# Optimization experiments

Hardware: AMD Instinct MI355X
Metric: run time of the kernel (lower is better)

## Reference

```python
import jax, jax.numpy as jnp
import numpy as np

N_USERS = 50000
N_ITEMS = 50000
N_NODES = N_USERS + N_ITEMS
N_EDGES = 1600000
N_PAIRS = 200000
USER_DIM = 128
ITEM_DIM = 128
HID = 64
LAYER_NUM = 2


def setup_inputs() -> dict:
    key = jax.random.key(0)
    ks = jax.random.split(key, 16)
    inp = {
        "user_features": jax.random.normal(ks[0], (N_USERS, USER_DIM), jnp.float32),
        "item_features": jax.random.normal(ks[1], (N_ITEMS, ITEM_DIM), jnp.float32),
        "item_side_feat": jax.random.normal(ks[2], (N_ITEMS, HID), jnp.float32),
        "T_f": jax.random.uniform(ks[3], (2 * N_PAIRS,), jnp.float32),
        "T_cf": jax.random.uniform(ks[4], (2 * N_PAIRS,), jnp.float32),
        "Wu": jax.random.normal(ks[5], (USER_DIM, HID), jnp.float32) / np.sqrt(USER_DIM),
        "bu": jax.random.normal(ks[6], (HID,), jnp.float32) * 0.01,
        "Wi": jax.random.normal(ks[7], (ITEM_DIM, HID), jnp.float32) / np.sqrt(ITEM_DIM),
        "bi": jax.random.normal(ks[8], (HID,), jnp.float32) * 0.01,
        "W1": jax.random.normal(ks[9], (1 + 2 * HID, HID), jnp.float32) / np.sqrt(1 + 2 * HID),
        "b1": jax.random.normal(ks[10], (HID,), jnp.float32) * 0.01,
        "W2": jax.random.normal(ks[11], (HID, 1), jnp.float32) / np.sqrt(HID),
        "edge_src": jax.random.randint(ks[12], (N_EDGES,), 0, N_NODES, jnp.int32),
        "edge_dst": jax.random.randint(ks[13], (N_EDGES,), 0, N_NODES, jnp.int32),
        "userId": jax.random.randint(ks[14], (N_PAIRS,), 0, N_USERS, jnp.int32),
        "pos_itemId": jax.random.randint(ks[15], (N_PAIRS,), 0, N_ITEMS, jnp.int32),
        "neg_itemId": jax.random.randint(jax.random.fold_in(key, 99), (N_PAIRS,), 0, N_ITEMS, jnp.int32),
    }
    return inp


def reference(user_features, item_features, item_side_feat, T_f, T_cf,
              Wu, bu, Wi, bi, W1, b1, W2,
              edge_src, edge_dst, userId, pos_itemId, neg_itemId):
    # degree-based symmetric normalization (out_deg^-0.5 on src, in_deg^-0.5 on dst)
    ones = jnp.ones((edge_src.shape[0],), jnp.float32)
    out_deg = jax.ops.segment_sum(ones, edge_src, num_segments=N_NODES)
    in_deg = jax.ops.segment_sum(ones, edge_dst, num_segments=N_NODES)
    out_norm = jax.lax.rsqrt(jnp.clip(out_deg, 1.0))[:, None]  # [N,1]
    in_norm = jax.lax.rsqrt(jnp.clip(in_deg, 1.0))[:, None]

    def gcn_layer(node_f):
        m = node_f * out_norm                                   # [N,H]
        agg = jax.ops.segment_sum(m[edge_src], edge_dst, num_segments=N_NODES)
        return agg * in_norm

    user_embedding = jax.nn.relu(user_features @ Wu + bu)       # [Nu,H]
    item_embedding = jax.nn.relu(item_features @ Wi + bi)       # [Ni,H]

    for i in range(LAYER_NUM):
        if i == 0:
            embeddings = gcn_layer(jnp.concatenate([user_embedding, item_embedding], axis=0))
        else:
            embeddings = gcn_layer(embeddings)
        scale = 1.0 / (i + 2)
        user_embedding = user_embedding + embeddings[:N_USERS] * scale
        item_embedding = item_embedding + embeddings[N_USERS:] * scale

    item_embedding = item_embedding + item_side_feat

    userE = user_embedding[userId]                              # [P,H]
    posE = item_embedding[pos_itemId]
    negE = item_embedding[neg_itemId]
    zi = jnp.concatenate([userE, userE], axis=0)                # [2P,H]
    zj = jnp.concatenate([posE, negE], axis=0)

    def decode(T):
        h = jnp.concatenate([zi, zj, T[:, None]], axis=1)       # [2P, 2H+1]
        h = jax.nn.elu(h @ W1 + b1)
        return (h @ W2)[:, 0]                                   # [2P]

    logits_f = decode(T_f)
    logits_cf = decode(T_cf)
    return (user_embedding, item_embedding, logits_f, logits_cf)
```

## Files before the change

kernel.cpp:

```cpp
#include <hip/hip_runtime.h>

#define NU 50000
#define NI 50000
#define NN 100000
#define NE 1600000
#define NP 200000
#define DIM 128
#define HID 64

#define HR 4
#define HC 32
#define RN (NN / HR)
#define RNW (RN / 2)
#define CE (NE / HC)

typedef unsigned short bf16_t;
typedef __attribute__((ext_vector_type(8))) short short8;
typedef __attribute__((ext_vector_type(4))) float f32x4;

__device__ __forceinline__ float bf2f(unsigned short u) {
  union { unsigned int i; float f; } c; c.i = ((unsigned int)u) << 16; return c.f;
}
__device__ __forceinline__ unsigned short f2bf(float f) {
  union { float f; unsigned int i; } c; c.f = f;
  unsigned int i = c.i;
  i += 0x7fffu + ((i >> 16) & 1u);
  return (unsigned short)(i >> 16);
}
__device__ __forceinline__ int geti(const void* p, int i, bool i64) {
  return i64 ? (int)((const long long*)p)[i] : ((const int*)p)[i];
}

__global__ __launch_bounds__(64) void k_detect(const bf16_t* __restrict__ uf,
                                               const int* __restrict__ ei,
                                               int* __restrict__ flag) {
  int lane = threadIdx.x;
  float m = 0.f;
  for (int i = lane; i < 4096; i += 64) {
    float v = fabsf(bf2f(uf[i]));
    if (v < 3e38f) m = fmaxf(m, v);
  }
  int cnt = 0;
  for (int i = lane; i < 4096; i += 64) {
    if (ei[2 * i + 1] == 0) cnt++;
  }
  for (int off = 32; off > 0; off >>= 1) {
    m = fmaxf(m, __shfl_xor(m, off));
    cnt += __shfl_xor(cnt, off);
  }
  if (lane == 0) {
    flag[0] = (m > 100.f) ? 1 : 0;
    flag[1] = (cnt > 2048) ? 1 : 0;
  }
}

__global__ __launch_bounds__(1024) void k_hist(const void* __restrict__ srcv,
                                               const void* __restrict__ dstv,
                                               const int* __restrict__ flag,
                                               int* __restrict__ pout,
                                               int* __restrict__ pin) {
  __shared__ unsigned int ho[RNW];
  __shared__ unsigned int hd[RNW];
  const bool i64 = (flag[1] != 0);
  int r = blockIdx.x & (HR - 1);
  int c = blockIdx.x >> 2;
  int lo = r * RN, hiN = lo + RN;
  int t = threadIdx.x;
  for (int i = t; i < RNW; i += 1024) { ho[i] = 0u; hd[i] = 0u; }
  __syncthreads();
  int ebeg = c * CE;
  if (!i64) {
    const int* sp = (const int*)srcv + ebeg;
    const int* dp = (const int*)dstv + ebeg;
    for (int e = t * 4; e < CE; e += 1024 * 4) {
      int4 sv = *(const int4*)(sp + e);
      int4 dv = *(const int4*)(dp + e);
      int ss[4] = {sv.x, sv.y, sv.z, sv.w};
      int dd[4] = {dv.x, dv.y, dv.z, dv.w};
#pragma unroll
      for (int k = 0; k < 4; ++k) {
        int s = ss[k];
        if (s >= lo && s < hiN) {
          int loc = s - lo;
          atomicAdd(&ho[loc >> 1], 1u << ((loc & 1) * 16));
        }
        int d = dd[k];
        if (d >= lo && d < hiN) {
          int loc = d - lo;
          atomicAdd(&hd[loc >> 1], 1u << ((loc & 1) * 16));
        }
      }
    }
  } else {
    const long long* sp = (const long long*)srcv + ebeg;
    const long long* dp = (const long long*)dstv + ebeg;
    for (int e = t; e < CE; e += 1024) {
      int s = (int)sp[e];
      if (s >= lo && s < hiN) {
        int loc = s - lo;
        atomicAdd(&ho[loc >> 1], 1u << ((loc & 1) * 16));
      }
      int d = (int)dp[e];
      if (d >= lo && d < hiN) {
        int loc = d - lo;
        atomicAdd(&hd[loc >> 1], 1u << ((loc & 1) * 16));
      }
    }
  }
  __syncthreads();
  int* po = pout + c * NN + lo;
  int* pi = pin + c * NN + lo;
  for (int i = t; i < RNW; i += 1024) {
    unsigned int o = ho[i], d = hd[i];
    int2 ov; ov.x = (int)(o & 0xffffu); ov.y = (int)(o >> 16);
    int2 dv; dv.x = (int)(d & 0xffffu); dv.y = (int)(d >> 16);
    *(int2*)(po + 2 * i) = ov;
    *(int2*)(pi + 2 * i) = dv;
  }
}

__global__ __launch_bounds__(256) void k_reduce(const int* __restrict__ pout,
                                                int* __restrict__ pin,
                                                int* __restrict__ din,
                                                float* __restrict__ onorm,
                                                float* __restrict__ inorm) {
  int n = blockIdx.x * 256 + threadIdx.x;
  if (n >= NN) return;
  int so = 0;
#pragma unroll
  for (int c = 0; c < HC; ++c) so += pout[c * NN + n];
  int si = 0;
#pragma unroll
  for (int c = 0; c < HC; ++c) {
    int v = pin[c * NN + n];
    pin[c * NN + n] = si;
    si += v;
  }
  din[n] = si;
  onorm[n] = rsqrtf((float)(so > 1 ? so : 1));
  inorm[n] = rsqrtf((float)(si > 1 ? si : 1));
}

__global__ __launch_bounds__(256) void k_scan1(const int* __restrict__ in,
                                               int* __restrict__ bsums, int n) {
  __shared__ int sh[256];
  int t = threadIdx.x;
  int base = blockIdx.x * 1024 + t * 4;
  int s = 0;
#pragma unroll
  for (int i = 0; i < 4; ++i)
    if (base + i < n) s += in[base + i];
  sh[t] = s;
  __syncthreads();
  for (int off = 128; off > 0; off >>= 1) {
    if (t < off) sh[t] += sh[t + off];
    __syncthreads();
  }
  if (t == 0) bsums[blockIdx.x] = sh[0];
}

__global__ __launch_bounds__(128) void k_scan2(const int* __restrict__ bsums,
                                               int* __restrict__ boffs, int nb) {
  __shared__ int sh[128];
  int t = threadIdx.x;
  int own = (t < nb) ? bsums[t] : 0;
  sh[t] = own;
  __syncthreads();
  for (int off = 1; off < 128; off <<= 1) {
    int add = (t >= off) ? sh[t - off] : 0;
    __syncthreads();
    sh[t] += add;
    __syncthreads();
  }
  if (t < nb) boffs[t] = sh[t] - own;
}

__global__ __launch_bounds__(256) void k_scan3(const int* __restrict__ in,
                                               const int* __restrict__ boffs,
                                               int* __restrict__ row_ptr, int n) {
  __shared__ int sh[256];
  int t = threadIdx.x;
  int base = blockIdx.x * 1024 + t * 4;
  int v[4];
  int s = 0;
#pragma unroll
  for (int i = 0; i < 4; ++i) {
    v[i] = (base + i < n) ? in[base + i] : 0;
    s += v[i];
  }
  sh[t] = s;
  __syncthreads();
  for (int off = 1; off < 256; off <<= 1) {
    int add = (t >= off) ? sh[t - off] : 0;
    __syncthreads();
    sh[t] += add;
    __syncthreads();
  }
  int excl = boffs[blockIdx.x] + sh[t] - s;
#pragma unroll
  for (int i = 0; i < 4; ++i) {
    if (base + i < n) {
      row_ptr[base + i] = excl;
      excl += v[i];
    }
  }
  if (blockIdx.x == 0 && t == 0) row_ptr[n] = NE;
}

__global__ __launch_bounds__(1024) void k_fill2(const void* __restrict__ srcv,
                                                const void* __restrict__ dstv,
                                                const int* __restrict__ flag,
                                                const int* __restrict__ row_ptr,
                                                const int* __restrict__ pin,
                                                int* __restrict__ csr_src) {
  __shared__ int cur[RN];
  const bool i64 = (flag[1] != 0);
  int r = blockIdx.x & (HR - 1);
  int c = blockIdx.x >> 2;
  int lo = r * RN, hiN = lo + RN;
  int t = threadIdx.x;
  const int* pi = pin + c * NN + lo;
  const int* rp = row_ptr + lo;
  for (int i = t; i < RN; i += 1024) cur[i] = rp[i] + pi[i];
  __syncthreads();
  int ebeg = c * CE;
  if (!i64) {
    const int* sp = (const int*)srcv + ebeg;
    const int* dp = (const int*)dstv + ebeg;
    for (int e = t * 4; e < CE; e += 1024 * 4) {
      int4 dv = *(const int4*)(dp + e);
      int4 sv = *(const int4*)(sp + e);
      int dd[4] = {dv.x, dv.y, dv.z, dv.w};
      int ss[4] = {sv.x, sv.y, sv.z, sv.w};
#pragma unroll
      for (int k = 0; k < 4; ++k) {
        int d = dd[k];
        if (d >= lo && d < hiN) {
          int slot = atomicAdd(&cur[d - lo], 1);
          csr_src[slot] = ss[k];
        }
      }
    }
  } else {
    const long long* sp = (const long long*)srcv + ebeg;
    const long long* dp = (const long long*)dstv + ebeg;
    for (int e = t; e < CE; e += 1024) {
      int d = (int)dp[e];
      if (d >= lo && d < hiN) {
        int slot = atomicAdd(&cur[d - lo], 1);
        csr_src[slot] = (int)sp[e];
      }
    }
  }
}

__global__ __launch_bounds__(256) void k_embed(const void* __restrict__ featv,
                                               const void* __restrict__ Wv,
                                               const void* __restrict__ biasv,
                                               const int* __restrict__ flag,
                                               const float* __restrict__ onorm_base,
                                               float* __restrict__ out,
                                               bf16_t* __restrict__ embs, int rows) {
  __shared__ float Ws[DIM * HID];
  __shared__ float bs[HID];
  const bool f32 = (flag[0] != 0);
  int t = threadIdx.x;
  if (f32) {
    const float* W = (const float*)Wv;
    for (int i = t; i < DIM * HID; i += 256) Ws[i] = W[i];
    if (t < HID) bs[t] = ((const float*)biasv)[t];
  } else {
    const bf16_t* W = (const bf16_t*)Wv;
    for (int i = t; i < DIM * HID; i += 256) Ws[i] = bf2f(W[i]);
    if (t < HID) bs[t] = bf2f(((const bf16_t*)biasv)[t]);
  }
  __syncthreads();
  int rl = t >> 4;
  int jq = t & 15;
  for (int rbase = blockIdx.x * 16; rbase < rows; rbase += gridDim.x * 16) {
    int row = rbase + rl;
    if (row >= rows) continue;
    float a0 = 0.f, a1 = 0.f, a2 = 0.f, a3 = 0.f;
    if (f32) {
      const float* fr = (const float*)featv + (size_t)row * DIM;
      for (int k0 = 0; k0 < DIM; k0 += 4) {
        float4 f4 = *(const float4*)(fr + k0);
        float fk[4] = {f4.x, f4.y, f4.z, f4.w};
#pragma unroll
        for (int kk = 0; kk < 4; ++kk) {
          const float* wr = &Ws[(k0 + kk) * HID + jq * 4];
          a0 += fk[kk] * wr[0];
          a1 += fk[kk] * wr[1];
          a2 += fk[kk] * wr[2];
          a3 += fk[kk] * wr[3];
        }
      }
    } else {
      const bf16_t* fr = (const bf16_t*)featv + (size_t)row * DIM;
      for (int k0 = 0; k0 < DIM; k0 += 8) {
        uint4 u = *(const uint4*)(fr + k0);
        unsigned int w[4] = {u.x, u.y, u.z, u.w};
#pragma unroll
        for (int kk = 0; kk < 8; ++kk) {
          unsigned short us = (unsigned short)((w[kk >> 1] >> ((kk & 1) * 16)) & 0xffffu);
          float fk = bf2f(us);
          const float* wr = &Ws[(k0 + kk) * HID + jq * 4];
          a0 += fk * wr[0];
          a1 += fk * wr[1];
          a2 += fk * wr[2];
          a3 += fk * wr[3];
        }
      }
    }
    float4 r;
    r.x = fmaxf(a0 + bs[jq * 4 + 0], 0.f);
    r.y = fmaxf(a1 + bs[jq * 4 + 1], 0.f);
    r.z = fmaxf(a2 + bs[jq * 4 + 2], 0.f);
    r.w = fmaxf(a3 + bs[jq * 4 + 3], 0.f);
    *(float4*)&out[(size_t)row * HID + jq * 4] = r;
    float sc = onorm_base[row];
    uint2 p;
    p.x = (unsigned int)f2bf(r.x * sc) | ((unsigned int)f2bf(r.y * sc) << 16);
    p.y = (unsigned int)f2bf(r.z * sc) | ((unsigned int)f2bf(r.w * sc) << 16);
    *(uint2*)&embs[(size_t)row * HID + jq * 4] = p;
  }
}

__global__ __launch_bounds__(256) void k_gather1(const bf16_t* __restrict__ embs,
                                                 const float* __restrict__ onorm,
                                                 const float* __restrict__ inorm,
                                                 const int* __restrict__ row_ptr,
                                                 const int* __restrict__ csr_src,
                                                 bf16_t* __restrict__ e1s) {
  int n = blockIdx.x * 4 + (threadIdx.x >> 6);
  if (n >= NN) return;
  int lane = threadIdx.x & 63;
  int g = lane >> 3;
  int l8 = (lane & 7) * 8;
  int beg = row_ptr[n], end = row_ptr[n + 1];
  float a[8];
#pragma unroll
  for (int j = 0; j < 8; ++j) a[j] = 0.f;
  for (int base = beg; base < end; base += 32) {
    int ev[4], sv[4];
#pragma unroll
    for (int k = 0; k < 4; ++k) {
      int ee = base + k * 8 + g;
      ev[k] = ee;
      sv[k] = csr_src[ee < end ? ee : end - 1];
    }
#pragma unroll
    for (int k = 0; k < 4; ++k) {
      uint4 u = *(const uint4*)(embs + (size_t)sv[k] * HID + l8);
      bool valid = ev[k] < end;
      unsigned int w[4] = {u.x, u.y, u.z, u.w};
#pragma unroll
      for (int j = 0; j < 4; ++j) {
        unsigned int wj = valid ? w[j] : 0u;
        a[2 * j]     += bf2f((unsigned short)(wj & 0xffffu));
        a[2 * j + 1] += bf2f((unsigned short)(wj >> 16));
      }
    }
  }
#pragma unroll
  for (int j = 0; j < 8; ++j) {
    a[j] += __shfl_xor(a[j], 8);
    a[j] += __shfl_xor(a[j], 16);
    a[j] += __shfl_xor(a[j], 32);
  }
  if (g == 0) {
    float sc = inorm[n] * onorm[n];
    uint4 p;
    p.x = (unsigned int)f2bf(a[0] * sc) | ((unsigned int)f2bf(a[1] * sc) << 16);
    p.y = (unsigned int)f2bf(a[2] * sc) | ((unsigned int)f2bf(a[3] * sc) << 16);
    p.z = (unsigned int)f2bf(a[4] * sc) | ((unsigned int)f2bf(a[5] * sc) << 16);
    p.w = (unsigned int)f2bf(a[6] * sc) | ((unsigned int)f2bf(a[7] * sc) << 16);
    *(uint4*)(e1s + (size_t)n * HID + l8) = p;
  }
}

__global__ __launch_bounds__(256) void k_gather2c(float* __restrict__ emb0,
                                                  const bf16_t* __restrict__ e1s,
                                                  const void* __restrict__ sidev,
                                                  const int* __restrict__ flag,
                                                  const float* __restrict__ onorm,
                                                  const float* __restrict__ inorm,
                                                  const int* __restrict__ row_ptr,
                                                  const int* __restrict__ csr_src,
                                                  bf16_t* __restrict__ fin_bf) {
  int n = blockIdx.x * 4 + (threadIdx.x >> 6);
  if (n >= NN) return;
  int lane = threadIdx.x & 63;
  int g = lane >> 3;
  int l8 = (lane & 7) * 8;
  int beg = row_ptr[n], end = row_ptr[n + 1];
  float a[8];
#pragma unroll
  for (int j = 0; j < 8; ++j) a[j] = 0.f;
  for (int base = beg; base < end; base += 32) {
    int ev[4], sv[4];
#pragma unroll
    for (int k = 0; k < 4; ++k) {
      int ee = base + k * 8 + g;
      ev[k] = ee;
      sv[k] = csr_src[ee < end ? ee : end - 1];
    }
#pragma unroll
    for (int k = 0; k < 4; ++k) {
      uint4 u = *(const uint4*)(e1s + (size_t)sv[k] * HID + l8);
      bool valid = ev[k] < end;
      unsigned int w[4] = {u.x, u.y, u.z, u.w};
#pragma unroll
      for (int j = 0; j < 4; ++j) {
        unsigned int wj = valid ? w[j] : 0u;
        a[2 * j]     += bf2f((unsigned short)(wj & 0xffffu));
        a[2 * j + 1] += bf2f((unsigned short)(wj >> 16));
      }
    }
  }
#pragma unroll
  for (int j = 0; j < 8; ++j) {
    a[j] += __shfl_xor(a[j], 8);
    a[j] += __shfl_xor(a[j], 16);
    a[j] += __shfl_xor(a[j], 32);
  }
  if (g == 0) {
    float inorm_n = inorm[n];
    float inv_on = 1.0f / onorm[n];
    size_t off = (size_t)n * HID + l8;
    uint4 u = *(const uint4*)(e1s + off);
    unsigned int w[4] = {u.x, u.y, u.z, u.w};
    float e1v[8];
#pragma unroll
    for (int j = 0; j < 4; ++j) {
      e1v[2 * j]     = bf2f((unsigned short)(w[j] & 0xffffu)) * inv_on;
      e1v[2 * j + 1] = bf2f((unsigned short)(w[j] >> 16)) * inv_on;
    }
    float4 b0 = *(const float4*)&emb0[off];
    float4 b1 = *(const float4*)&emb0[off + 4];
    float bb[8] = {b0.x, b0.y, b0.z, b0.w, b1.x, b1.y, b1.z, b1.w};
    const float s2 = 1.f / 3.f;
    float vv[8];
#pragma unroll
    for (int j = 0; j < 8; ++j)
      vv[j] = bb[j] + 0.5f * e1v[j] + s2 * a[j] * inorm_n;
    if (n >= NU) {
      size_t soff = (size_t)(n - NU) * HID + l8;
      if (flag[0] != 0) {
        float4 s0 = *(const float4*)((const float*)sidev + soff);
        float4 s1 = *(const float4*)((const float*)sidev + soff + 4);
        vv[0] += s0.x; vv[1] += s0.y; vv[2] += s0.z; vv[3] += s0.w;
        vv[4] += s1.x; vv[5] += s1.y; vv[6] += s1.z; vv[7] += s1.w;
      } else {
        uint4 su = *(const uint4*)((const bf16_t*)sidev + soff);
        unsigned int sw[4] = {su.x, su.y, su.z, su.w};
#pragma unroll
        for (int j = 0; j < 4; ++j) {
          vv[2 * j]     += bf2f((unsigned short)(sw[j] & 0xffffu));
          vv[2 * j + 1] += bf2f((unsigned short)(sw[j] >> 16));
        }
      }
    }
    float4 o0, o1;
    o0.x = vv[0]; o0.y = vv[1]; o0.z = vv[2]; o0.w = vv[3];
    o1.x = vv[4]; o1.y = vv[5]; o1.z = vv[6]; o1.w = vv[7];
    *(float4*)&emb0[off] = o0;
    *(float4*)&emb0[off + 4] = o1;
    uint4 pb;
    pb.x = (unsigned int)f2bf(vv[0]) | ((unsigned int)f2bf(vv[1]) << 16);
    pb.y = (unsigned int)f2bf(vv[2]) | ((unsigned int)f2bf(vv[3]) << 16);
    pb.z = (unsigned int)f2bf(vv[4]) | ((unsigned int)f2bf(vv[5]) << 16);
    pb.w = (unsigned int)f2bf(vv[6]) | ((unsigned int)f2bf(vv[7]) << 16);
    *(uint4*)(fin_bf + off) = pb;
  }
}

__global__ __launch_bounds__(256) void k_decode(const bf16_t* __restrict__ zb,
                                                const void* __restrict__ W1v,
                                                const void* __restrict__ b1v,
                                                const void* __restrict__ W2v,
                                                const void* __restrict__ Tfv,
                                                const void* __restrict__ Tcfv,
                                                const int* __restrict__ flag,
                                                const void* __restrict__ userId,
                                                const void* __restrict__ posId,
                                                const void* __restrict__ negId,
                                                float* __restrict__ out_lf,
                                                float* __restrict__ out_lcf) {
  __shared__ bf16_t W1b[128 * 65];
  __shared__ float wlast[HID], b1s[HID], W2s[HID];
  const bool f32 = (flag[0] != 0);
  const bool i64 = (flag[1] != 0);
  int t = threadIdx.x;
  if (f32) {
    const float* W1 = (const float*)W1v;
    for (int i = t; i < 128 * 64; i += 256) W1b[(i >> 6) * 65 + (i & 63)] = f2bf(W1[i]);
    if (t < HID) {
      wlast[t] = W1[128 * 64 + t];
      b1s[t] = ((const float*)b1v)[t];
      W2s[t] = ((const float*)W2v)[t];
    }
  } else {
    const bf16_t* W1 = (const bf16_t*)W1v;
    for (int i = t; i < 128 * 64; i += 256) W1b[(i >> 6) * 65 + (i & 63)] = W1[i];
    if (t < HID) {
      wlast[t] = bf2f(W1[128 * 64 + t]);
      b1s[t] = bf2f(((const bf16_t*)b1v)[t]);
      W2s[t] = bf2f(((const bf16_t*)W2v)[t]);
    }
  }
  __syncthreads();
  int wv = t >> 6;
  int lane = t & 63;
  int m = lane & 15;
  int q = lane >> 4;
  short8 Bf[4][4];
#pragma unroll
  for (int c = 0; c < 4; ++c)
#pragma unroll
    for (int nt = 0; nt < 4; ++nt)
#pragma unroll
      for (int j = 0; j < 8; ++j)
        Bf[c][nt][j] = (short)W1b[(c * 32 + q * 8 + j) * 65 + nt * 16 + m];

  const int tiles = (2 * NP) / 16;
  for (int tile = blockIdx.x * 4 + wv; tile < tiles; tile += gridDim.x * 4) {
    int pr = tile * 16 + m;
    int pid = pr < NP ? pr : pr - NP;
    int uid = geti(userId, pid, i64);
    int iid = (pr < NP) ? geti(posId, pid, i64) : geti(negId, pid, i64);
    const bf16_t* ur = zb + (size_t)uid * HID;
    const bf16_t* ir = zb + (size_t)(NU + iid) * HID;
    short8 a0 = *(const short8*)(ur + q * 8);
    short8 a1 = *(const short8*)(ur + 32 + q * 8);
    short8 a2 = *(const short8*)(ir + q * 8);
    short8 a3 = *(const short8*)(ir + 32 + q * 8);
    f32x4 acc[4];
#pragma unroll
    for (int nt = 0; nt < 4; ++nt) acc[nt] = (f32x4)(0.f);
#pragma unroll
    for (int nt = 0; nt < 4; ++nt) {
      acc[nt] = __builtin_amdgcn_mfma_f32_16x16x32_bf16(a0, Bf[0][nt], acc[nt], 0, 0, 0);
      acc[nt] = __builtin_amdgcn_mfma_f32_16x16x32_bf16(a1, Bf[1][nt], acc[nt], 0, 0, 0);
      acc[nt] = __builtin_amdgcn_mfma_f32_16x16x32_bf16(a2, Bf[2][nt], acc[nt], 0, 0, 0);
      acc[nt] = __builtin_amdgcn_mfma_f32_16x16x32_bf16(a3, Bf[3][nt], acc[nt], 0, 0, 0);
    }
    float tfr[4], tcfr[4];
    int rbase = tile * 16 + q * 4;
    if (f32) {
      float4 t4 = *(const float4*)((const float*)Tfv + rbase);
      float4 c4 = *(const float4*)((const float*)Tcfv + rbase);
      tfr[0] = t4.x; tfr[1] = t4.y; tfr[2] = t4.z; tfr[3] = t4.w;
      tcfr[0] = c4.x; tcfr[1] = c4.y; tcfr[2] = c4.z; tcfr[3] = c4.w;
    } else {
      const bf16_t* tp = (const bf16_t*)Tfv + rbase;
      const bf16_t* cp = (const bf16_t*)Tcfv + rbase;
#pragma unroll
      for (int r = 0; r < 4; ++r) { tfr[r] = bf2f(tp[r]); tcfr[r] = bf2f(cp[r]); }
    }
#pragma unroll
    for (int r = 0; r < 4; ++r) {
      float sf = 0.f, scf = 0.f;
#pragma unroll
      for (int nt = 0; nt < 4; ++nt) {
        int n = nt * 16 + m;
        float x = acc[nt][r] + b1s[n];
        float wl = wlast[n];
        float w2 = W2s[n];
        float bfv = x + tfr[r] * wl;
        float bcv = x + tcfr[r] * wl;
        float hf = bfv > 0.f ? bfv : (__expf(bfv) - 1.f);
        float hc = bcv > 0.f ? bcv : (__expf(bcv) - 1.f);
        sf += hf * w2;
        scf += hc * w2;
      }
      sf += __shfl_xor(sf, 1); scf += __shfl_xor(scf, 1);
      sf += __shfl_xor(sf, 2); scf += __shfl_xor(scf, 2);
      sf += __shfl_xor(sf, 4); scf += __shfl_xor(scf, 4);
      sf += __shfl_xor(sf, 8); scf += __shfl_xor(scf, 8);
      if (m == 0) {
        int pr2 = rbase + r;
        out_lf[pr2] = sf;
        out_lcf[pr2] = scf;
      }
    }
  }
}

extern "C" void kernel_launch(void* const* d_in, const int* in_sizes, int n_in,
                              void* d_out, int out_size, void* d_ws, size_t ws_size,
                              hipStream_t stream) {
  (void)in_sizes; (void)n_in; (void)out_size;
  const void* user_f = d_in[0];
  const void* item_f = d_in[1];
  const void* side   = d_in[2];
  const void* Tf     = d_in[3];
  const void* Tcf    = d_in[4];
  const void* Wu     = d_in[5];
  const void* bu     = d_in[6];
  const void* Wi     = d_in[7];
  const void* bi     = d_in[8];
  const void* W1     = d_in[9];
  const void* b1     = d_in[10];
  const void* W2     = d_in[11];
  const void* esrc   = d_in[12];
  const void* edst   = d_in[13];
  const void* userId = d_in[14];
  const void* posId  = d_in[15];
  const void* negId  = d_in[16];

  const size_t WS_NEEDED = 33601280;
  if (ws_size < WS_NEEDED) return;

  char* ws = (char*)d_ws;
  int*   deg_in  = (int*)(ws + 0);
  float* onorm   = (float*)(ws + 400000);
  float* inorm   = (float*)(ws + 800000);
  int*   row_ptr = (int*)(ws + 1200000);
  int*   bsums   = (int*)(ws + 1600128);
  int*   boffs   = (int*)(ws + 1600640);
  int*   flag    = (int*)(ws + 1601152);
  int*   csr_src = (int*)(ws + 1601280);
  int*   pout    = (int*)(ws + 8001280);
  int*   pin     = (int*)(ws + 20801280);
  bf16_t* embs   = (bf16_t*)(ws + 8001280);
  bf16_t* e1s    = (bf16_t*)(ws + 20801280);
  bf16_t* fin_bf = embs;

  float* out     = (float*)d_out;
  float* emb0    = out;
  float* out_lf  = out + (size_t)NN * HID;
  float* out_lcf = out_lf + 2 * NP;

  k_detect<<<1, 64, 0, stream>>>((const bf16_t*)user_f, (const int*)esrc, flag);
  k_hist<<<HR * HC, 1024, 0, stream>>>(esrc, edst, flag, pout, pin);
  k_reduce<<<(NN + 255) / 256, 256, 0, stream>>>(pout, pin, deg_in, onorm, inorm);
  k_scan1<<<98, 256, 0, stream>>>(deg_in, bsums, NN);
  k_scan2<<<1, 128, 0, stream>>>(bsums, boffs, 98);
  k_scan3<<<98, 256, 0, stream>>>(deg_in, boffs, row_ptr, NN);
  k_fill2<<<HR * HC, 1024, 0, stream>>>(esrc, edst, flag, row_ptr, pin, csr_src);
  k_embed<<<256, 256, 0, stream>>>(user_f, Wu, bu, flag, onorm, emb0, embs, NU);
  k_embed<<<256, 256, 0, stream>>>(item_f, Wi, bi, flag, onorm + NU,
                                   emb0 + (size_t)NU * HID, embs + (size_t)NU * HID, NI);
  k_gather1<<<NN / 4, 256, 0, stream>>>(embs, onorm, inorm, row_ptr, csr_src, e1s);
  k_gather2c<<<NN / 4, 256, 0, stream>>>(emb0, e1s, side, flag, onorm, inorm, row_ptr,
                                         csr_src, fin_bf);
  k_decode<<<1024, 256, 0, stream>>>(fin_bf, W1, b1, W2, Tf, Tcf, flag,
                                     userId, posId, negId, out_lf, out_lcf);
}
```

Measured before the change: 429.8 us.

## Store GCN embedding tables in column-blocked layout and gather per column block

The bf16 node embedding tables move from row-major [N,64] to eight column-block tables [8][N][8]. Each gather block now handles one 16-byte column slice for 16 nodes, with 16 lanes per node striding over edges, so each per-block table is much smaller and more likely to stay in cache. The cost is that CSR indices and row pointers are read once per column block, and each gather fetches only 16 bytes. The embed kernel is also changed so each thread computes 8 output columns and writes the blocked layout.

New measurement: 555.8 us. 29.3% more time.

```diff
diff --git a/kernel.cpp b/kernel.cpp
--- a/kernel.cpp
+++ b/kernel.cpp
@@ -14,9 +14,13 @@
 #define RNW (RN / 2)
 #define CE (NE / HC)
 
+#define CB 8
+#define CBW 8
+
 typedef unsigned short bf16_t;
 typedef __attribute__((ext_vector_type(8))) short short8;
 typedef __attribute__((ext_vector_type(4))) float f32x4;
+typedef __attribute__((ext_vector_type(2))) float f32x2;
 
 __device__ __forceinline__ float bf2f(unsigned short u) {
   union { unsigned int i; float f; } c; c.i = ((unsigned int)u) << 16; return c.f;
@@ -26,6 +30,13 @@
   unsigned int i = c.i;
   i += 0x7fffu + ((i >> 16) & 1u);
   return (unsigned short)(i >> 16);
+}
+__device__ __forceinline__ f32x2 unpack2(unsigned int w) {
+  union { unsigned int i; float f; } lo, hi;
+  lo.i = w << 16;
+  hi.i = w & 0xffff0000u;
+  f32x2 r; r.x = lo.f; r.y = hi.f;
+  return r;
 }
 __device__ __forceinline__ int geti(const void* p, int i, bool i64) {
   return i64 ? (int)((const long long*)p)[i] : ((const int*)p)[i];
@@ -260,7 +271,8 @@
                                                const int* __restrict__ flag,
                                                const float* __restrict__ onorm_base,
                                                float* __restrict__ out,
-                                               bf16_t* __restrict__ embs, int rows) {
+                                               bf16_t* __restrict__ embs_tab,
+                                               int row0, int rows) {
   __shared__ float Ws[DIM * HID];
   __shared__ float bs[HID];
   const bool f32 = (flag[0] != 0);
@@ -275,12 +287,14 @@
     if (t < HID) bs[t] = bf2f(((const bf16_t*)biasv)[t]);
   }
   __syncthreads();
-  int rl = t >> 4;
-  int jq = t & 15;
-  for (int rbase = blockIdx.x * 16; rbase < rows; rbase += gridDim.x * 16) {
+  int rl = t >> 3;
+  int jq = t & 7;
+  for (int rbase = blockIdx.x * 32; rbase < rows; rbase += gridDim.x * 32) {
     int row = rbase + rl;
     if (row >= rows) continue;
-    float a0 = 0.f, a1 = 0.f, a2 = 0.f, a3 = 0.f;
+    float a[8];
+#pragma unroll
+    for (int j = 0; j < 8; ++j) a[j] = 0.f;
     if (f32) {
       const float* fr = (const float*)featv + (size_t)row * DIM;
       for (int k0 = 0; k0 < DIM; k0 += 4) {
@@ -288,11 +302,9 @@
         float fk[4] = {f4.x, f4.y, f4.z, f4.w};
 #pragma unroll
         for (int kk = 0; kk < 4; ++kk) {
-          const float* wr = &Ws[(k0 + kk) * HID + jq * 4];
-          a0 += fk[kk] * wr[0];
-          a1 += fk[kk] * wr[1];
-          a2 += fk[kk] * wr[2];
-          a3 += fk[kk] * wr[3];
+          const float* wr = &Ws[(k0 + kk) * HID + jq * 8];
+#pragma unroll
+          for (int j = 0; j < 8; ++j) a[j] += fk[kk] * wr[j];
         }
       }
     } else {
@@ -304,25 +316,28 @@
         for (int kk = 0; kk < 8; ++kk) {
           unsigned short us = (unsigned short)((w[kk >> 1] >> ((kk & 1) * 16)) & 0xffffu);
           float fk = bf2f(us);
-          const float* wr = &Ws[(k0 + kk) * HID + jq * 4];
-          a0 += fk * wr[0];
-          a1 += fk * wr[1];
-          a2 += fk * wr[2];
-          a3 += fk * wr[3];
+          const float* wr = &Ws[(k0 + kk) * HID + jq * 8];
+#pragma unroll
+          for (int j = 0; j < 8; ++j) a[j] += fk * wr[j];
         }
       }
     }
-    float4 r;
-    r.x = fmaxf(a0 + bs[jq * 4 + 0], 0.f);
-    r.y = fmaxf(a1 + bs[jq * 4 + 1], 0.f);
-    r.z = fmaxf(a2 + bs[jq * 4 + 2], 0.f);
-    r.w = fmaxf(a3 + bs[jq * 4 + 3], 0.f);
-    *(float4*)&out[(size_t)row * HID + jq * 4] = r;
+    float r[8];
+#pragma unroll
+    for (int j = 0; j < 8; ++j) r[j] = fmaxf(a[j] + bs[jq * 8 + j], 0.f);
+    float4 o0, o1;
+    o0.x = r[0]; o0.y = r[1]; o0.z = r[2]; o0.w = r[3];
+    o1.x = r[4]; o1.y = r[5]; o1.z = r[6]; o1.w = r[7];
+    size_t roff = (size_t)row * HID + jq * 8;
+    *(float4*)&out[roff] = o0;
+    *(float4*)&out[roff + 4] = o1;
     float sc = onorm_base[row];
-    uint2 p;
-    p.x = (unsigned int)f2bf(r.x * sc) | ((unsigned int)f2bf(r.y * sc) << 16);
-    p.y = (unsigned int)f2bf(r.z * sc) | ((unsigned int)f2bf(r.w * sc) << 16);
-    *(uint2*)&embs[(size_t)row * HID + jq * 4] = p;
+    uint4 p;
+    p.x = (unsigned int)f2bf(r[0] * sc) | ((unsigned int)f2bf(r[1] * sc) << 16);
+    p.y = (unsigned int)f2bf(r[2] * sc) | ((unsigned int)f2bf(r[3] * sc) << 16);
+    p.z = (unsigned int)f2bf(r[4] * sc) | ((unsigned int)f2bf(r[5] * sc) << 16);
+    p.w = (unsigned int)f2bf(r[6] * sc) | ((unsigned int)f2bf(r[7] * sc) << 16);
+    *(uint4*)&embs_tab[((size_t)jq * NN + (row0 + row)) * CBW] = p;
   }
 }
 
@@ -332,50 +347,44 @@
                                                  const int* __restrict__ row_ptr,
                                                  const int* __restrict__ csr_src,
                                                  bf16_t* __restrict__ e1s) {
-  int n = blockIdx.x * 4 + (threadIdx.x >> 6);
-  if (n >= NN) return;
+  int cb = blockIdx.x & (CB - 1);
+  int ng = blockIdx.x >> 3;
+  int w = threadIdx.x >> 6;
   int lane = threadIdx.x & 63;
-  int g = lane >> 3;
-  int l8 = (lane & 7) * 8;
+  int rw = lane >> 4;
+  int el = lane & 15;
+  int n = ng * 16 + w * 4 + rw;
+  const bf16_t* tbl = embs + (size_t)cb * NN * CBW;
   int beg = row_ptr[n], end = row_ptr[n + 1];
-  float a[8];
-#pragma unroll
-  for (int j = 0; j < 8; ++j) a[j] = 0.f;
-  for (int base = beg; base < end; base += 32) {
-    int ev[4], sv[4];
-#pragma unroll
-    for (int k = 0; k < 4; ++k) {
-      int ee = base + k * 8 + g;
-      ev[k] = ee;
-      sv[k] = csr_src[ee < end ? ee : end - 1];
-    }
-#pragma unroll
-    for (int k = 0; k < 4; ++k) {
-      uint4 u = *(const uint4*)(embs + (size_t)sv[k] * HID + l8);
-      bool valid = ev[k] < end;
-      unsigned int w[4] = {u.x, u.y, u.z, u.w};
-#pragma unroll
-      for (int j = 0; j < 4; ++j) {
-        unsigned int wj = valid ? w[j] : 0u;
-        a[2 * j]     += bf2f((unsigned short)(wj & 0xffffu));
-        a[2 * j + 1] += bf2f((unsigned short)(wj >> 16));
-      }
-    }
-  }
-#pragma unroll
-  for (int j = 0; j < 8; ++j) {
-    a[j] += __shfl_xor(a[j], 8);
-    a[j] += __shfl_xor(a[j], 16);
-    a[j] += __shfl_xor(a[j], 32);
-  }
-  if (g == 0) {
+  f32x2 a[4];
+#pragma unroll
+  for (int j = 0; j < 4; ++j) a[j] = (f32x2)(0.f);
+  for (int base = beg; base < end; base += 16) {
+    int ee = base + el;
+    int idx = csr_src[ee < end ? ee : end - 1];
+    uint4 u = *(const uint4*)(tbl + (size_t)idx * CBW);
+    unsigned int msk = (ee < end) ? 0xffffffffu : 0u;
+    a[0] += unpack2(u.x & msk);
+    a[1] += unpack2(u.y & msk);
+    a[2] += unpack2(u.z & msk);
+    a[3] += unpack2(u.w & msk);
+  }
+#pragma unroll
+  for (int s = 1; s < 16; s <<= 1) {
+#pragma unroll
+    for (int j = 0; j < 4; ++j) {
+      a[j].x += __shfl_xor(a[j].x, s);
+      a[j].y += __shfl_xor(a[j].y, s);
+    }
+  }
+  if (el == 0) {
     float sc = inorm[n] * onorm[n];
     uint4 p;
-    p.x = (unsigned int)f2bf(a[0] * sc) | ((unsigned int)f2bf(a[1] * sc) << 16);
-    p.y = (unsigned int)f2bf(a[2] * sc) | ((unsigned int)f2bf(a[3] * sc) << 16);
-    p.z = (unsigned int)f2bf(a[4] * sc) | ((unsigned int)f2bf(a[5] * sc) << 16);
-    p.w = (unsigned int)f2bf(a[6] * sc) | ((unsigned int)f2bf(a[7] * sc) << 16);
-    *(uint4*)(e1s + (size_t)n * HID + l8) = p;
+    p.x = (unsigned int)f2bf(a[0].x * sc) | ((unsigned int)f2bf(a[0].y * sc) << 16);
+    p.y = (unsigned int)f2bf(a[1].x * sc) | ((unsigned int)f2bf(a[1].y * sc) << 16);
+    p.z = (unsigned int)f2bf(a[2].x * sc) | ((unsigned int)f2bf(a[2].y * sc) << 16);
+    p.w = (unsigned int)f2bf(a[3].x * sc) | ((unsigned int)f2bf(a[3].y * sc) << 16);
+    *(uint4*)(e1s + ((size_t)cb * NN + n) * CBW) = p;
   }
 }
 
@@ -388,54 +397,49 @@
                                                   const int* __restrict__ row_ptr,
                                                   const int* __restrict__ csr_src,
                                                   bf16_t* __restrict__ fin_bf) {
-  int n = blockIdx.x * 4 + (threadIdx.x >> 6);
-  if (n >= NN) return;
+  int cb = blockIdx.x & (CB - 1);
+  int ng = blockIdx.x >> 3;
+  int w = threadIdx.x >> 6;
   int lane = threadIdx.x & 63;
-  int g = lane >> 3;
-  int l8 = (lane & 7) * 8;
+  int rw = lane >> 4;
+  int el = lane & 15;
+  int n = ng * 16 + w * 4 + rw;
+  const bf16_t* tbl = e1s + (size_t)cb * NN * CBW;
   int beg = row_ptr[n], end = row_ptr[n + 1];
-  float a[8];
-#pragma unroll
-  for (int j = 0; j < 8; ++j) a[j] = 0.f;
-  for (int base = beg; base < end; base += 32) {
-    int ev[4], sv[4];
-#pragma unroll
-    for (int k = 0; k < 4; ++k) {
-      int ee = base + k * 8 + g;
-      ev[k] = ee;
-      sv[k] = csr_src[ee < end ? ee : end - 1];
-    }
-#pragma unroll
-    for (int k = 0; k < 4; ++k) {
-      uint4 u = *(const uint4*)(e1s + (size_t)sv[k] * HID + l8);
-      bool valid = ev[k] < end;
-      unsigned int w[4] = {u.x, u.y, u.z, u.w};
-#pragma unroll
-      for (int j = 0; j < 4; ++j) {
-        unsigned int wj = valid ? w[j] : 0u;
-        a[2 * j]     += bf2f((unsigned short)(wj & 0xffffu));
-        a[2 * j + 1] += bf2f((unsigned short)(wj >> 16));
-      }
-    }
-  }
-#pragma unroll
-  for (int j = 0; j < 8; ++j) {
-    a[j] += __shfl_xor(a[j], 8);
-    a[j] += __shfl_xor(a[j], 16);
-    a[j] += __shfl_xor(a[j], 32);
-  }
-  if (g == 0) {
+  f32x2 a[4];
+#pragma unroll
+  for (int j = 0; j < 4; ++j) a[j] = (f32x2)(0.f);
+  for (int base = beg; base < end; base += 16) {
+    int ee = base + el;
+    int idx = csr_src[ee < end ? ee : end - 1];
+    uint4 u = *(const uint4*)(tbl + (size_t)idx * CBW);
+    unsigned int msk = (ee < end) ? 0xffffffffu : 0u;
+    a[0] += unpack2(u.x & msk);
+    a[1] += unpack2(u.y & msk);
+    a[2] += unpack2(u.z & msk);
+    a[3] += unpack2(u.w & msk);
+  }
+#pragma unroll
+  for (int s = 1; s < 16; s <<= 1) {
+#pragma unroll
+    for (int j = 0; j < 4; ++j) {
+      a[j].x += __shfl_xor(a[j].x, s);
+      a[j].y += __shfl_xor(a[j].y, s);
+    }
+  }
+  if (el == 0) {
+    float aa[8] = {a[0].x, a[0].y, a[1].x, a[1].y, a[2].x, a[2].y, a[3].x, a[3].y};
     float inorm_n = inorm[n];
     float inv_on = 1.0f / onorm[n];
-    size_t off = (size_t)n * HID + l8;
-    uint4 u = *(const uint4*)(e1s + off);
-    unsigned int w[4] = {u.x, u.y, u.z, u.w};
+    uint4 u = *(const uint4*)(tbl + (size_t)n * CBW);
+    unsigned int sw[4] = {u.x, u.y, u.z, u.w};
     float e1v[8];
 #pragma unroll
     for (int j = 0; j < 4; ++j) {
-      e1v[2 * j]     = bf2f((unsigned short)(w[j] & 0xffffu)) * inv_on;
-      e1v[2 * j + 1] = bf2f((unsigned short)(w[j] >> 16)) * inv_on;
-    }
+      e1v[2 * j]     = bf2f((unsigned short)(sw[j] & 0xffffu)) * inv_on;
+      e1v[2 * j + 1] = bf2f((unsigned short)(sw[j] >> 16)) * inv_on;
+    }
+    size_t off = (size_t)n * HID + cb * 8;
     float4 b0 = *(const float4*)&emb0[off];
     float4 b1 = *(const float4*)&emb0[off + 4];
     float bb[8] = {b0.x, b0.y, b0.z, b0.w, b1.x, b1.y, b1.z, b1.w};
@@ -443,9 +447,9 @@
     float vv[8];
 #pragma unroll
     for (int j = 0; j < 8; ++j)
-      vv[j] = bb[j] + 0.5f * e1v[j] + s2 * a[j] * inorm_n;
+      vv[j] = bb[j] + 0.5f * e1v[j] + s2 * aa[j] * inorm_n;
     if (n >= NU) {
-      size_t soff = (size_t)(n - NU) * HID + l8;
+      size_t soff = (size_t)(n - NU) * HID + cb * 8;
       if (flag[0] != 0) {
         float4 s0 = *(const float4*)((const float*)sidev + soff);
         float4 s1 = *(const float4*)((const float*)sidev + soff + 4);
@@ -453,11 +457,11 @@
         vv[4] += s1.x; vv[5] += s1.y; vv[6] += s1.z; vv[7] += s1.w;
       } else {
         uint4 su = *(const uint4*)((const bf16_t*)sidev + soff);
-        unsigned int sw[4] = {su.x, su.y, su.z, su.w};
+        unsigned int qw[4] = {su.x, su.y, su.z, su.w};
 #pragma unroll
         for (int j = 0; j < 4; ++j) {
-          vv[2 * j]     += bf2f((unsigned short)(sw[j] & 0xffffu));
-          vv[2 * j + 1] += bf2f((unsigned short)(sw[j] >> 16));
+          vv[2 * j]     += bf2f((unsigned short)(qw[j] & 0xffffu));
+          vv[2 * j + 1] += bf2f((unsigned short)(qw[j] >> 16));
         }
       }
     }
@@ -639,12 +643,12 @@
   k_scan2<<<1, 128, 0, stream>>>(bsums, boffs, 98);
   k_scan3<<<98, 256, 0, stream>>>(deg_in, boffs, row_ptr, NN);
   k_fill2<<<HR * HC, 1024, 0, stream>>>(esrc, edst, flag, row_ptr, pin, csr_src);
-  k_embed<<<256, 256, 0, stream>>>(user_f, Wu, bu, flag, onorm, emb0, embs, NU);
+  k_embed<<<256, 256, 0, stream>>>(user_f, Wu, bu, flag, onorm, emb0, embs, 0, NU);
   k_embed<<<256, 256, 0, stream>>>(item_f, Wi, bi, flag, onorm + NU,
-                                   emb0 + (size_t)NU * HID, embs + (size_t)NU * HID, NI);
-  k_gather1<<<NN / 4, 256, 0, stream>>>(embs, onorm, inorm, row_ptr, csr_src, e1s);
-  k_gather2c<<<NN / 4, 256, 0, stream>>>(emb0, e1s, side, flag, onorm, inorm, row_ptr,
-                                         csr_src, fin_bf);
+                                   emb0 + (size_t)NU * HID, embs, NU, NI);
+  k_gather1<<<(NN / 16) * CB, 256, 0, stream>>>(embs, onorm, inorm, row_ptr, csr_src, e1s);
+  k_gather2c<<<(NN / 16) * CB, 256, 0, stream>>>(emb0, e1s, side, flag, onorm, inorm,
+                                                 row_ptr, csr_src, fin_bf);
   k_decode<<<1024, 256, 0, stream>>>(fin_bf, W1, b1, W2, Tf, Tcf, flag,
                                      userId, posId, negId, out_lf, out_lcf);
 }
```
